# Performance work log

Hardware: AMD Instinct MI355X
Metric: run time of the kernel (lower is better)

## Reference

```python
import jax, jax.numpy as jnp
import numpy as np

N = 100000
E = 1600000
F_IN = 128
H = 128


def setup_inputs() -> dict:
    key = jax.random.key(0)
    ks = jax.random.split(key, 12)
    x = jax.random.normal(ks[0], (N, F_IN), dtype=jnp.float32)
    edge_index = jax.random.randint(ks[1], (2, E), 0, N, dtype=jnp.int64)
    s = 1.0 / np.sqrt(F_IN)
    sh = 1.0 / np.sqrt(H)
    inp = {"x": x, "edge_index": edge_index}
    # SAGEConv params: lin_l (neighbor agg, with bias), lin_r (root, no bias)
    inp["W1l"] = jax.random.uniform(ks[2], (H, F_IN), jnp.float32, -s, s)
    inp["b1"] = jnp.zeros((H,), jnp.float32)
    inp["W1r"] = jax.random.uniform(ks[3], (H, F_IN), jnp.float32, -s, s)
    inp["W2l"] = jax.random.uniform(ks[4], (H, H), jnp.float32, -sh, sh)
    inp["b2"] = jnp.zeros((H,), jnp.float32)
    inp["W2r"] = jax.random.uniform(ks[5], (H, H), jnp.float32, -sh, sh)
    inp["W3l"] = jax.random.uniform(ks[6], (H, H), jnp.float32, -sh, sh)
    inp["b3"] = jnp.zeros((H,), jnp.float32)
    inp["W3r"] = jax.random.uniform(ks[7], (H, H), jnp.float32, -sh, sh)
    inp["Wo"] = jax.random.uniform(ks[8], (1, H), jnp.float32, -sh, sh)
    inp["bo"] = jnp.zeros((1,), jnp.float32)
    return inp


def _sage_max(h, src, dst, Wl, bl, Wr):
    # max-aggregate source features at destination nodes (empty -> 0, as PyG)
    m = jax.ops.segment_max(h[src], dst, num_segments=N)  # [N, d]
    m = jnp.where(jnp.isfinite(m), m, jnp.zeros_like(m))
    return m @ Wl.T + bl + h @ Wr.T


def reference(x, edge_index, W1l, b1, W1r, W2l, b2, W2r, W3l, b3, W3r, Wo, bo):
    src, dst = edge_index[0], edge_index[1]
    h1 = jax.nn.elu(_sage_max(x, src, dst, W1l, b1, W1r))
    h2 = jax.nn.elu(_sage_max(h1, src, dst, W2l, b2, W2r)) + h1
    h3 = jax.nn.elu(_sage_max(h2, src, dst, W3l, b3, W3r)) + h2
    return jax.nn.sigmoid(h3 @ Wo.T + bo)  # [N, 1]
```

## Files before the change

### kernel.cpp

```cpp
#include <hip/hip_runtime.h>
#include <hip/hip_fp16.h>
#include <math.h>

#define HDIM 128

#define BSHIFT 7
#define BW 128
#define BCAP 4096
#define NBKMAX 1024
#define CHUNK 4096

typedef __attribute__((ext_vector_type(8))) _Float16 f16x8;
typedef __attribute__((ext_vector_type(2))) _Float16 f16x2;
typedef __attribute__((ext_vector_type(16))) float f32x16;
typedef unsigned int uint32;
typedef unsigned short u16;

__device__ __forceinline__ uint32 hmax2u(uint32 a, uint32 b) {
    f16x2 ha = __builtin_bit_cast(f16x2, a);
    f16x2 hb = __builtin_bit_cast(f16x2, b);
    f16x2 r = __builtin_elementwise_max(ha, hb);
    return __builtin_bit_cast(uint32, r);
}
__device__ __forceinline__ uint32 hadd2u(uint32 a, uint32 b) {
    f16x2 ha = __builtin_bit_cast(f16x2, a);
    f16x2 hb = __builtin_bit_cast(f16x2, b);
    f16x2 r = ha + hb;
    return __builtin_bit_cast(uint32, r);
}


__global__ __launch_bounds__(256) void bucket_bin(
    const int* __restrict__ ei, int E_, int nbk,
    int* __restrict__ bucketCnt, uint32* __restrict__ tmp)
{
    __shared__ int cnt[NBKMAX];
    __shared__ int gbase[NBKMAX];
    const int t = threadIdx.x;
    const int start = blockIdx.x * CHUNK;
    const int end = min(start + CHUNK, E_);

    for (int i = t; i < nbk; i += 256) cnt[i] = 0;
    __syncthreads();
    for (int e = start + t; e < end; e += 256)
        atomicAdd(&cnt[ei[E_ + e] >> BSHIFT], 1);
    __syncthreads();
    for (int i = t; i < nbk; i += 256) {
        int c = cnt[i];
        gbase[i] = c ? atomicAdd(&bucketCnt[i], c) : 0;
    }
    __syncthreads();
    for (int i = t; i < nbk; i += 256) cnt[i] = 0;
    __syncthreads();
    for (int e = start + t; e < end; e += 256) {
        int d = ei[E_ + e];
        int s = ei[e];
        int b = d >> BSHIFT;
        int r = atomicAdd(&cnt[b], 1);
        tmp[(size_t)b * BCAP + gbase[b] + r] =
            ((uint32)(d & (BW - 1)) << 17) | (uint32)s;
    }
}

__global__ __launch_bounds__(1024) void bucket_scan(
    const int* __restrict__ bucketCnt, int* __restrict__ bucketBase,
    int nbk, int* __restrict__ off, int N_, int E_) {
    __shared__ int sd[1024];
    int t = threadIdx.x;
    int v = (t < nbk) ? bucketCnt[t] : 0;
    sd[t] = v;
    __syncthreads();
    for (int ofs = 1; ofs < 1024; ofs <<= 1) {
        int add = (t >= ofs) ? sd[t - ofs] : 0;
        __syncthreads();
        sd[t] += add;
        __syncthreads();
    }
    if (t < nbk) bucketBase[t] = sd[t] - v;
    if (t == 0) off[N_] = E_;
}

__global__ __launch_bounds__(256) void bucket_csr(
    const uint32* __restrict__ tmp, const int* __restrict__ bucketCnt,
    const int* __restrict__ bucketBase,
    int* __restrict__ off, int* __restrict__ srcs, int N_)
{
    __shared__ int lc[BW];
    __shared__ int lo[BW];
    __shared__ int sd[256];
    const int b = blockIdx.x, t = threadIdx.x;
    const int cnt = bucketCnt[b], base = bucketBase[b];
    const uint32* tp = tmp + (size_t)b * BCAP;

    if (t < BW) lc[t] = 0;
    __syncthreads();
    for (int i = t; i < cnt; i += 256) atomicAdd(&lc[tp[i] >> 17], 1);
    __syncthreads();

    int v = (t < BW) ? lc[t] : 0;
    sd[t] = v;
    __syncthreads();
    for (int ofs = 1; ofs < 256; ofs <<= 1) {
        int add = (t >= ofs) ? sd[t - ofs] : 0;
        __syncthreads();
        sd[t] += add;
        __syncthreads();
    }
    if (t < BW) lo[t] = sd[t] - v;
    __syncthreads();

    for (int i = t; i < BW; i += 256) {
        int node = b * BW + i;
        if (node < N_) off[node] = base + lo[i];
    }
    if (t < BW) lc[t] = lo[t];
    __syncthreads();
    for (int i = t; i < cnt; i += 256) {
        uint32 p = tp[i];
        int dl = p >> 17, s = p & 0x1FFFF;
        int pos = base + atomicAdd(&lc[dl], 1);
        srcs[pos] = s;
    }
}


__global__ void cast_x(const float* __restrict__ x, uint32* __restrict__ xb, int n2) {
    int i = blockIdx.x * 256 + threadIdx.x;
    if (i >= n2) return;
    float2 v = ((const float2*)x)[i];
    f16x2 h = { (_Float16)v.x, (_Float16)v.y };
    xb[i] = __builtin_bit_cast(uint32, h);
}

__global__ void cast_weights_packed(
    const float* __restrict__ W1l, const float* __restrict__ W1r,
    const float* __restrict__ W2l, const float* __restrict__ W2r,
    const float* __restrict__ W3l, const float* __restrict__ W3r,
    f16x8* __restrict__ PW)
{
    int tid = blockIdx.x * 256 + threadIdx.x;
    if (tid >= 3 * 4096) return;
    int layer = tid >> 12, rem = tid & 4095;
    int g = rem >> 10, ks = (rem >> 6) & 15, lane = rem & 63;
    int col = g * 32 + (lane & 31), kq = lane >> 5;
    const float* src;
    if (layer == 0)      src = (ks < 8) ? W1l : W1r;
    else if (layer == 1) src = (ks < 8) ? W2l : W2r;
    else                 src = (ks < 8) ? W3l : W3r;
    int kk = (ks & 7) * 16 + kq * 8;
    f16x8 v;
#pragma unroll
    for (int j = 0; j < 8; ++j) v[j] = (_Float16)src[col * HDIM + kk + j];
    PW[tid] = v;
}


__global__ __launch_bounds__(256) void gather_max(
    const uint32* __restrict__ hb,
    uint32* __restrict__ mb,
    const int* __restrict__ off, const int* __restrict__ srcs, int n_nodes)
{
    const int w = threadIdx.x >> 6, lane = threadIdx.x & 63;
    const int node = blockIdx.x * 4 + w;
    if (node >= n_nodes) return;
    const int es = lane >> 4, ch = lane & 15;
    const int e0 = off[node], e1 = off[node + 1];
    const uint4* hp = (const uint4*)hb;

    const uint32 NINF = 0xFC00FC00u;
    uint32 m0 = NINF, m1 = NINF, m2 = NINF, m3 = NINF;

    int e = e0 + es;
    for (; e + 12 < e1; e += 16) {
        int s0 = srcs[e], s1 = srcs[e + 4], s2 = srcs[e + 8], s3 = srcs[e + 12];
        uint4 v0 = hp[(size_t)s0 * 16 + ch];
        uint4 v1 = hp[(size_t)s1 * 16 + ch];
        uint4 v2 = hp[(size_t)s2 * 16 + ch];
        uint4 v3 = hp[(size_t)s3 * 16 + ch];
        m0 = hmax2u(m0, v0.x); m1 = hmax2u(m1, v0.y);
        m2 = hmax2u(m2, v0.z); m3 = hmax2u(m3, v0.w);
        m0 = hmax2u(m0, v1.x); m1 = hmax2u(m1, v1.y);
        m2 = hmax2u(m2, v1.z); m3 = hmax2u(m3, v1.w);
        m0 = hmax2u(m0, v2.x); m1 = hmax2u(m1, v2.y);
        m2 = hmax2u(m2, v2.z); m3 = hmax2u(m3, v2.w);
        m0 = hmax2u(m0, v3.x); m1 = hmax2u(m1, v3.y);
        m2 = hmax2u(m2, v3.z); m3 = hmax2u(m3, v3.w);
    }
    for (; e < e1; e += 4) {
        uint4 v0 = hp[(size_t)srcs[e] * 16 + ch];
        m0 = hmax2u(m0, v0.x); m1 = hmax2u(m1, v0.y);
        m2 = hmax2u(m2, v0.z); m3 = hmax2u(m3, v0.w);
    }

    m0 = hmax2u(m0, __shfl_xor(m0, 16)); m0 = hmax2u(m0, __shfl_xor(m0, 32));
    m1 = hmax2u(m1, __shfl_xor(m1, 16)); m1 = hmax2u(m1, __shfl_xor(m1, 32));
    m2 = hmax2u(m2, __shfl_xor(m2, 16)); m2 = hmax2u(m2, __shfl_xor(m2, 32));
    m3 = hmax2u(m3, __shfl_xor(m3, 16)); m3 = hmax2u(m3, __shfl_xor(m3, 32));

    if (es == 0) {
        uint4 r = make_uint4(0u, 0u, 0u, 0u);
        if (e1 > e0) { r.x = m0; r.y = m1; r.z = m2; r.w = m3; }
        ((uint4*)mb)[(size_t)node * 16 + ch] = r;
    }
}


#define ESTRIDE 136

__global__ __launch_bounds__(256) void gemm_layer(
    const uint4* __restrict__ mb, const uint4* __restrict__ hb,
    const uint4* __restrict__ res, uint4* __restrict__ outb,
    const uint4* __restrict__ PW,
    const float* __restrict__ bias, int n_nodes)
{
    __shared__ uint4 sm[512];
    __shared__ uint4 sh[512];
    __shared__ _Float16 ho[32 * ESTRIDE];
    const int t = threadIdx.x, lane = t & 63, w = t >> 6;
    const int base = blockIdx.x * 32;
    const int l31 = lane & 31, kq = lane >> 5;

#pragma unroll
    for (int r = 0; r < 2; ++r) {
        int g = r * 256 + t;
        int row = g >> 4, ch = g & 15;
        int sw = ch ^ (row & 7);
        size_t gi = (size_t)(base + row) * 16 + ch;
        sm[row * 16 + sw] = mb[gi];
        sh[row * 16 + sw] = hb[gi];
    }
    __syncthreads();

    f32x16 acc = {};

#pragma unroll
    for (int k = 0; k < 8; ++k) {
        f16x8 a = __builtin_bit_cast(f16x8, sm[l31 * 16 + ((2 * k + kq) ^ (l31 & 7))]);
        f16x8 b = __builtin_bit_cast(f16x8, PW[(w * 16 + k) * 64 + lane]);
        acc = __builtin_amdgcn_mfma_f32_32x32x16_f16(a, b, acc, 0, 0, 0);
    }
#pragma unroll
    for (int k = 0; k < 8; ++k) {
        f16x8 a = __builtin_bit_cast(f16x8, sh[l31 * 16 + ((2 * k + kq) ^ (l31 & 7))]);
        f16x8 b = __builtin_bit_cast(f16x8, PW[(w * 16 + 8 + k) * 64 + lane]);
        acc = __builtin_amdgcn_mfma_f32_32x32x16_f16(a, b, acc, 0, 0, 0);
    }

    const int C = w * 32 + l31;
    const float bv = bias[C];
#pragma unroll
    for (int r = 0; r < 16; ++r) {
        int row = (r & 3) + 8 * (r >> 2) + 4 * kq;
        float v = acc[r] + bv;
        v = (v > 0.f) ? v : (__expf(v) - 1.f);
        ho[row * ESTRIDE + C] = (_Float16)v;
    }
    __syncthreads();

#pragma unroll
    for (int r = 0; r < 2; ++r) {
        int g = r * 256 + t;
        int row = g >> 4, ch = g & 15;
        int R = base + row;
        if (R >= n_nodes) continue;
        uint4 v = *(const uint4*)&ho[row * ESTRIDE + ch * 8];
        if (res) {
            uint4 rv = res[(size_t)R * 16 + ch];
            v.x = hadd2u(v.x, rv.x); v.y = hadd2u(v.y, rv.y);
            v.z = hadd2u(v.z, rv.z); v.w = hadd2u(v.w, rv.w);
        }
        outb[(size_t)R * 16 + ch] = v;
    }
}


__global__ __launch_bounds__(256) void readout(
    const uint32* __restrict__ h, const float* __restrict__ Wo,
    const float* __restrict__ bo, float* __restrict__ out, int n_nodes)
{
    int t = threadIdx.x;
    int n = t >> 4, l = t & 15;
    int node = blockIdx.x * 16 + n;
    if (node >= n_nodes) return;
    float s = 0.f;
    for (int j = l; j < 64; j += 16) {
        uint32 v = h[(size_t)node * 64 + j];
        f16x2 hh = __builtin_bit_cast(f16x2, v);
        s += (float)hh.x * Wo[2 * j] + (float)hh.y * Wo[2 * j + 1];
    }
    for (int o = 8; o; o >>= 1) s += __shfl_down(s, o, 16);
    if (l == 0) out[node] = 1.f / (1.f + expf(-(s + bo[0])));
}


extern "C" void kernel_launch(void* const* d_in, const int* in_sizes, int n_in,
                              void* d_out, int out_size, void* d_ws, size_t ws_size,
                              hipStream_t stream) {
    const float* x   = (const float*)d_in[0];
    const int*   ei  = (const int*)d_in[1];
    const float* W1l = (const float*)d_in[2];
    const float* b1  = (const float*)d_in[3];
    const float* W1r = (const float*)d_in[4];
    const float* W2l = (const float*)d_in[5];
    const float* b2  = (const float*)d_in[6];
    const float* W2r = (const float*)d_in[7];
    const float* W3l = (const float*)d_in[8];
    const float* b3  = (const float*)d_in[9];
    const float* W3r = (const float*)d_in[10];
    const float* Wo  = (const float*)d_in[11];
    const float* bo  = (const float*)d_in[12];
    float* out = (float*)d_out;

    const int N_ = in_sizes[0] / HDIM;
    const int E_ = in_sizes[1] / 2;
    const int Np = (N_ + 127) & ~127;
    const int nbk = (N_ + BW - 1) / BW;

    size_t o = 0;
    auto carve = [&](size_t bytes) { size_t r = o; o = (o + bytes + 255) & ~255ULL; return r; };
    char* ws = (char*)d_ws;
    int* off        = (int*)(ws + carve((size_t)(N_ + 1) * 4));
    int* bucketCnt  = (int*)(ws + carve((size_t)NBKMAX * 4));
    int* bucketBase = (int*)(ws + carve((size_t)NBKMAX * 4));
    int* srcs       = (int*)(ws + carve((size_t)E_ * 4));
    uint32* tmp     = (uint32*)(ws + carve((size_t)nbk * BCAP * 4));
    uint4* PW       = (uint4*)(ws + carve((size_t)3 * 4096 * 16));
    uint32* XB      = (uint32*)(ws + carve((size_t)Np * 64 * 4));
    uint32* H1B     = (uint32*)(ws + carve((size_t)Np * 64 * 4));
    uint32* MB      = (uint32*)(ws + carve((size_t)Np * 64 * 4));
    (void)ws_size; (void)n_in; (void)out_size;

    (void)hipMemsetAsync(bucketCnt, 0, (size_t)NBKMAX * 4, stream);
    bucket_bin<<<(E_ + CHUNK - 1) / CHUNK, 256, 0, stream>>>(ei, E_, nbk, bucketCnt, tmp);
    bucket_scan<<<1, 1024, 0, stream>>>(bucketCnt, bucketBase, nbk, off, N_, E_);
    bucket_csr<<<nbk, 256, 0, stream>>>(tmp, bucketCnt, bucketBase, off, srcs, N_);

    cast_weights_packed<<<(3 * 4096 + 255) / 256, 256, 0, stream>>>(
        W1l, W1r, W2l, W2r, W3l, W3r, (f16x8*)PW);
    cast_x<<<(N_ * 64 + 255) / 256, 256, 0, stream>>>(x, XB, N_ * 64);

    const int nbG = (N_ + 3) / 4;
    const int nbM = Np / 32;

    const uint4* PW1 = PW;
    const uint4* PW2 = PW + 4096;
    const uint4* PW3 = PW + 8192;

    gather_max<<<nbG, 256, 0, stream>>>(XB, MB, off, srcs, N_);
    gemm_layer<<<nbM, 256, 0, stream>>>((const uint4*)MB, (const uint4*)XB, nullptr,
                                        (uint4*)H1B, PW1, b1, N_);
    gather_max<<<nbG, 256, 0, stream>>>(H1B, MB, off, srcs, N_);
    gemm_layer<<<nbM, 256, 0, stream>>>((const uint4*)MB, (const uint4*)H1B, (const uint4*)H1B,
                                        (uint4*)XB, PW2, b2, N_);
    gather_max<<<nbG, 256, 0, stream>>>(XB, MB, off, srcs, N_);
    gemm_layer<<<nbM, 256, 0, stream>>>((const uint4*)MB, (const uint4*)XB, (const uint4*)XB,
                                        (uint4*)H1B, PW3, b3, N_);

    readout<<<(N_ + 15) / 16, 256, 0, stream>>>(H1B, Wo, bo, out, N_);
}
```

Baseline: 398.9 us.

## Fuse max-gather, GEMM and readout into one per-layer kernel

```diff
diff --git a/kernel.cpp b/kernel.cpp
--- a/kernel.cpp
+++ b/kernel.cpp
@@ -155,84 +155,80 @@
 }
 
 
-__global__ __launch_bounds__(256) void gather_max(
+#define ESTRIDE 136
+
+__global__ __launch_bounds__(256, 8) void fused_layer(
     const uint32* __restrict__ hb,
-    uint32* __restrict__ mb,
-    const int* __restrict__ off, const int* __restrict__ srcs, int n_nodes)
+    const int* __restrict__ off, const int* __restrict__ srcs,
+    uint4* __restrict__ outb,
+    const uint4* __restrict__ PW,
+    const float* __restrict__ bias,
+    int use_res,
+    const float* __restrict__ Wo, const float* __restrict__ bo,
+    float* __restrict__ out, int n_nodes)
 {
-    const int w = threadIdx.x >> 6, lane = threadIdx.x & 63;
-    const int node = blockIdx.x * 4 + w;
-    if (node >= n_nodes) return;
-    const int es = lane >> 4, ch = lane & 15;
-    const int e0 = off[node], e1 = off[node + 1];
-    const uint4* hp = (const uint4*)hb;
-
-    const uint32 NINF = 0xFC00FC00u;
-    uint32 m0 = NINF, m1 = NINF, m2 = NINF, m3 = NINF;
-
-    int e = e0 + es;
-    for (; e + 12 < e1; e += 16) {
-        int s0 = srcs[e], s1 = srcs[e + 4], s2 = srcs[e + 8], s3 = srcs[e + 12];
-        uint4 v0 = hp[(size_t)s0 * 16 + ch];
-        uint4 v1 = hp[(size_t)s1 * 16 + ch];
-        uint4 v2 = hp[(size_t)s2 * 16 + ch];
-        uint4 v3 = hp[(size_t)s3 * 16 + ch];
-        m0 = hmax2u(m0, v0.x); m1 = hmax2u(m1, v0.y);
-        m2 = hmax2u(m2, v0.z); m3 = hmax2u(m3, v0.w);
-        m0 = hmax2u(m0, v1.x); m1 = hmax2u(m1, v1.y);
-        m2 = hmax2u(m2, v1.z); m3 = hmax2u(m3, v1.w);
-        m0 = hmax2u(m0, v2.x); m1 = hmax2u(m1, v2.y);
-        m2 = hmax2u(m2, v2.z); m3 = hmax2u(m3, v2.w);
-        m0 = hmax2u(m0, v3.x); m1 = hmax2u(m1, v3.y);
-        m2 = hmax2u(m2, v3.z); m3 = hmax2u(m3, v3.w);
-    }
-    for (; e < e1; e += 4) {
-        uint4 v0 = hp[(size_t)srcs[e] * 16 + ch];
-        m0 = hmax2u(m0, v0.x); m1 = hmax2u(m1, v0.y);
-        m2 = hmax2u(m2, v0.z); m3 = hmax2u(m3, v0.w);
-    }
-
-    m0 = hmax2u(m0, __shfl_xor(m0, 16)); m0 = hmax2u(m0, __shfl_xor(m0, 32));
-    m1 = hmax2u(m1, __shfl_xor(m1, 16)); m1 = hmax2u(m1, __shfl_xor(m1, 32));
-    m2 = hmax2u(m2, __shfl_xor(m2, 16)); m2 = hmax2u(m2, __shfl_xor(m2, 32));
-    m3 = hmax2u(m3, __shfl_xor(m3, 16)); m3 = hmax2u(m3, __shfl_xor(m3, 32));
-
-    if (es == 0) {
-        uint4 r = make_uint4(0u, 0u, 0u, 0u);
-        if (e1 > e0) { r.x = m0; r.y = m1; r.z = m2; r.w = m3; }
-        ((uint4*)mb)[(size_t)node * 16 + ch] = r;
-    }
-}
-
-
-#define ESTRIDE 136
-
-__global__ __launch_bounds__(256) void gemm_layer(
-    const uint4* __restrict__ mb, const uint4* __restrict__ hb,
-    const uint4* __restrict__ res, uint4* __restrict__ outb,
-    const uint4* __restrict__ PW,
-    const float* __restrict__ bias, int n_nodes)
-{
-    __shared__ uint4 sm[512];
+    __shared__ alignas(16) char smemA[32 * ESTRIDE * 2];
     __shared__ uint4 sh[512];
-    __shared__ _Float16 ho[32 * ESTRIDE];
+    uint4*     sm = (uint4*)smemA;
+    _Float16*  ho = (_Float16*)smemA;
+
     const int t = threadIdx.x, lane = t & 63, w = t >> 6;
     const int base = blockIdx.x * 32;
     const int l31 = lane & 31, kq = lane >> 5;
+    const uint4* hp = (const uint4*)hb;
 
 #pragma unroll
     for (int r = 0; r < 2; ++r) {
         int g = r * 256 + t;
-        int row = g >> 4, ch = g & 15;
-        int sw = ch ^ (row & 7);
-        size_t gi = (size_t)(base + row) * 16 + ch;
-        sm[row * 16 + sw] = mb[gi];
-        sh[row * 16 + sw] = hb[gi];
+        int row = g >> 4, c = g & 15;
+        sh[row * 16 + (c ^ (row & 7))] = hp[(size_t)(base + row) * 16 + c];
+    }
+
+    const int es = lane >> 4, ch = lane & 15;
+    const uint32 NINF = 0xFC00FC00u;
+    for (int i = 0; i < 8; ++i) {
+        const int row = w * 8 + i;
+        const int node = base + row;
+        int e0 = 0, e1 = 0;
+        if (node < n_nodes) { e0 = off[node]; e1 = off[node + 1]; }
+        uint32 m0 = NINF, m1 = NINF, m2 = NINF, m3 = NINF;
+
+        int e = e0 + es;
+        for (; e + 12 < e1; e += 16) {
+            int s0 = srcs[e], s1 = srcs[e + 4], s2 = srcs[e + 8], s3 = srcs[e + 12];
+            uint4 v0 = hp[(size_t)s0 * 16 + ch];
+            uint4 v1 = hp[(size_t)s1 * 16 + ch];
+            uint4 v2 = hp[(size_t)s2 * 16 + ch];
+            uint4 v3 = hp[(size_t)s3 * 16 + ch];
+            m0 = hmax2u(m0, v0.x); m1 = hmax2u(m1, v0.y);
+            m2 = hmax2u(m2, v0.z); m3 = hmax2u(m3, v0.w);
+            m0 = hmax2u(m0, v1.x); m1 = hmax2u(m1, v1.y);
+            m2 = hmax2u(m2, v1.z); m3 = hmax2u(m3, v1.w);
+            m0 = hmax2u(m0, v2.x); m1 = hmax2u(m1, v2.y);
+            m2 = hmax2u(m2, v2.z); m3 = hmax2u(m3, v2.w);
+            m0 = hmax2u(m0, v3.x); m1 = hmax2u(m1, v3.y);
+            m2 = hmax2u(m2, v3.z); m3 = hmax2u(m3, v3.w);
+        }
+        for (; e < e1; e += 4) {
+            uint4 v0 = hp[(size_t)srcs[e] * 16 + ch];
+            m0 = hmax2u(m0, v0.x); m1 = hmax2u(m1, v0.y);
+            m2 = hmax2u(m2, v0.z); m3 = hmax2u(m3, v0.w);
+        }
+
+        m0 = hmax2u(m0, __shfl_xor(m0, 16)); m0 = hmax2u(m0, __shfl_xor(m0, 32));
+        m1 = hmax2u(m1, __shfl_xor(m1, 16)); m1 = hmax2u(m1, __shfl_xor(m1, 32));
+        m2 = hmax2u(m2, __shfl_xor(m2, 16)); m2 = hmax2u(m2, __shfl_xor(m2, 32));
+        m3 = hmax2u(m3, __shfl_xor(m3, 16)); m3 = hmax2u(m3, __shfl_xor(m3, 32));
+
+        if (es == 0) {
+            uint4 rr = make_uint4(0u, 0u, 0u, 0u);
+            if (e1 > e0) { rr.x = m0; rr.y = m1; rr.z = m2; rr.w = m3; }
+            sm[row * 16 + (ch ^ (row & 7))] = rr;
+        }
     }
     __syncthreads();
 
     f32x16 acc = {};
-
 #pragma unroll
     for (int k = 0; k < 8; ++k) {
         f16x8 a = __builtin_bit_cast(f16x8, sm[l31 * 16 + ((2 * k + kq) ^ (l31 & 7))]);
@@ -245,6 +241,8 @@
         f16x8 b = __builtin_bit_cast(f16x8, PW[(w * 16 + 8 + k) * 64 + lane]);
         acc = __builtin_amdgcn_mfma_f32_32x32x16_f16(a, b, acc, 0, 0, 0);
     }
+
+    __syncthreads();
 
     const int C = w * 32 + l31;
     const float bv = bias[C];
@@ -260,36 +258,33 @@
 #pragma unroll
     for (int r = 0; r < 2; ++r) {
         int g = r * 256 + t;
-        int row = g >> 4, ch = g & 15;
+        int row = g >> 4, c = g & 15;
         int R = base + row;
-        if (R >= n_nodes) continue;
-        uint4 v = *(const uint4*)&ho[row * ESTRIDE + ch * 8];
-        if (res) {
-            uint4 rv = res[(size_t)R * 16 + ch];
+        bool valid = (R < n_nodes);
+        uint4 v = *(const uint4*)&ho[row * ESTRIDE + c * 8];
+        if (use_res) {
+            uint4 rv = sh[row * 16 + (c ^ (row & 7))];
             v.x = hadd2u(v.x, rv.x); v.y = hadd2u(v.y, rv.y);
             v.z = hadd2u(v.z, rv.z); v.w = hadd2u(v.w, rv.w);
         }
-        outb[(size_t)R * 16 + ch] = v;
-    }
-}
-
-
-__global__ __launch_bounds__(256) void readout(
-    const uint32* __restrict__ h, const float* __restrict__ Wo,
-    const float* __restrict__ bo, float* __restrict__ out, int n_nodes)
-{
-    int t = threadIdx.x;
-    int n = t >> 4, l = t & 15;
-    int node = blockIdx.x * 16 + n;
-    if (node >= n_nodes) return;
-    float s = 0.f;
-    for (int j = l; j < 64; j += 16) {
-        uint32 v = h[(size_t)node * 64 + j];
-        f16x2 hh = __builtin_bit_cast(f16x2, v);
-        s += (float)hh.x * Wo[2 * j] + (float)hh.y * Wo[2 * j + 1];
-    }
-    for (int o = 8; o; o >>= 1) s += __shfl_down(s, o, 16);
-    if (l == 0) out[node] = 1.f / (1.f + expf(-(s + bo[0])));
+        if (outb) {
+            if (valid) outb[(size_t)R * 16 + c] = v;
+        } else {
+            const float* wo = Wo + c * 8;
+            f16x2 a0 = __builtin_bit_cast(f16x2, v.x);
+            f16x2 a1 = __builtin_bit_cast(f16x2, v.y);
+            f16x2 a2 = __builtin_bit_cast(f16x2, v.z);
+            f16x2 a3 = __builtin_bit_cast(f16x2, v.w);
+            float s = (float)a0.x * wo[0] + (float)a0.y * wo[1]
+                    + (float)a1.x * wo[2] + (float)a1.y * wo[3]
+                    + (float)a2.x * wo[4] + (float)a2.y * wo[5]
+                    + (float)a3.x * wo[6] + (float)a3.y * wo[7];
+#pragma unroll
+            for (int o = 8; o; o >>= 1) s += __shfl_down(s, o, 16);
+            if (valid && (t & 15) == 0)
+                out[R] = 1.f / (1.f + expf(-(s + bo[0])));
+        }
+    }
 }
 
 
@@ -327,7 +322,6 @@
     uint4* PW       = (uint4*)(ws + carve((size_t)3 * 4096 * 16));
     uint32* XB      = (uint32*)(ws + carve((size_t)Np * 64 * 4));
     uint32* H1B     = (uint32*)(ws + carve((size_t)Np * 64 * 4));
-    uint32* MB      = (uint32*)(ws + carve((size_t)Np * 64 * 4));
     (void)ws_size; (void)n_in; (void)out_size;
 
     (void)hipMemsetAsync(bucketCnt, 0, (size_t)NBKMAX * 4, stream);
@@ -339,22 +333,16 @@
         W1l, W1r, W2l, W2r, W3l, W3r, (f16x8*)PW);
     cast_x<<<(N_ * 64 + 255) / 256, 256, 0, stream>>>(x, XB, N_ * 64);
 
-    const int nbG = (N_ + 3) / 4;
-    const int nbM = Np / 32;
+    const int nbF = (N_ + 31) / 32;
 
     const uint4* PW1 = PW;
     const uint4* PW2 = PW + 4096;
     const uint4* PW3 = PW + 8192;
 
-    gather_max<<<nbG, 256, 0, stream>>>(XB, MB, off, srcs, N_);
-    gemm_layer<<<nbM, 256, 0, stream>>>((const uint4*)MB, (const uint4*)XB, nullptr,
-                                        (uint4*)H1B, PW1, b1, N_);
-    gather_max<<<nbG, 256, 0, stream>>>(H1B, MB, off, srcs, N_);
-    gemm_layer<<<nbM, 256, 0, stream>>>((const uint4*)MB, (const uint4*)H1B, (const uint4*)H1B,
-                                        (uint4*)XB, PW2, b2, N_);
-    gather_max<<<nbG, 256, 0, stream>>>(XB, MB, off, srcs, N_);
-    gemm_layer<<<nbM, 256, 0, stream>>>((const uint4*)MB, (const uint4*)XB, (const uint4*)XB,
-                                        (uint4*)H1B, PW3, b3, N_);
-
-    readout<<<(N_ + 15) / 16, 256, 0, stream>>>(H1B, Wo, bo, out, N_);
-}
+    fused_layer<<<nbF, 256, 0, stream>>>(XB, off, srcs, (uint4*)H1B, PW1, b1,
+                                         0, nullptr, nullptr, nullptr, N_);
+    fused_layer<<<nbF, 256, 0, stream>>>(H1B, off, srcs, (uint4*)XB, PW2, b2,
+                                         1, nullptr, nullptr, nullptr, N_);
+    fused_layer<<<nbF, 256, 0, stream>>>(XB, off, srcs, nullptr, PW3, b3,
+                                         1, Wo, bo, out, N_);
+}
```

Result: faster. 376.1 us (-5.7%).
